# Performance work log

Measured on AMD Instinct MI355X. Metric: run time of the kernel, lower is better.

The kernel has to match this reference:

```python
import jax, jax.numpy as jnp
import numpy as np

KSIZE, STRIDE, RATE, FUSE_K, SCALE = 3, 1, 2, 3, 10.0
ESCAPE_NAN = 1e-4


def same_pad(x, k, s):
    # torch same_padding: pad so out = ceil(in/s)
    H, W = x.shape[2], x.shape[3]
    oh, ow = -(-H // s), -(-W // s)
    ph = max(0, (oh - 1) * s + k - H)
    pw = max(0, (ow - 1) * s + k - W)
    return jnp.pad(x, ((0, 0), (0, 0), (ph // 2, ph - ph // 2), (pw // 2, pw - pw // 2)))


def extract_patches(x, k, s):
    # torch Unfold -> view(B,C,k,k,L) -> permute(0,4,1,2,3): returns [B, L, C, k, k]
    x = same_pad(x, k, s)
    B, C, H, W = x.shape
    oh, ow = (H - k) // s + 1, (W - k) // s + 1
    rows = jnp.arange(oh)[:, None] * s + jnp.arange(k)[None, :]
    cols = jnp.arange(ow)[:, None] * s + jnp.arange(k)[None, :]
    p = x[:, :, rows][:, :, :, :, cols]  # [B,C,oh,k,ow,k]
    return p.transpose(0, 2, 4, 1, 3, 5).reshape(B, oh * ow, C, k, k)


def conv1x1(x, w, b):
    return jnp.einsum('bchw,oc->bohw', x, w) + b[None, :, None, None]


def conv2d(x, w):
    return jax.lax.conv_general_dilated(x, w, (1, 1), 'VALID',
                                        dimension_numbers=('NCHW', 'OIHW', 'NCHW'))


def conv_transpose2d(x, w, stride, pad):
    # matches F.conv_transpose2d(x, w[Cin,Cout,k,k], stride, padding=pad)
    k = w.shape[2]
    wf = jnp.flip(w, (2, 3))
    return jax.lax.conv_general_dilated(x, wf, (1, 1), [(k - 1 - pad, k - 1 - pad)] * 2,
                                        lhs_dilation=(stride, stride),
                                        dimension_numbers=('NCHW', 'IOHW', 'NCHW'))


def global_attention(a, bm, c, wq, bq, wk, bk, wv, bv, gamma):
    # a,bm: [B,C,H,W]; c: [B,1,Hc,Wc]; mask scales score rows before softmax
    B, C, H, W = a.shape
    dr = c.shape[2] // H
    c = c[:, :, ::dr, ::dr]  # nearest downsample, matches F.interpolate(mode='nearest')
    q = conv1x1(a, wq, bq).reshape(B, C, H * W)
    k = conv1x1(bm, wk, bk).reshape(B, C, H * W)
    sim = jnp.einsum('bci,bcj->bij', q, k)  # [B,N,N]
    mv = c.reshape(B, H * W)
    attn = jax.nn.softmax(sim * mv[:, :, None], axis=-1)
    v = conv1x1(a, wv, bv).reshape(B, C, H * W)
    out = jnp.einsum('bcj,bij->bci', v, attn).reshape(B, C, H, W)
    return gamma * a * c + (1.0 - c) * out


def _forward(f, b, mask, fa, pa):
    B, C, H, W = b.shape
    kernel = 2 * RATE
    raw_w = extract_patches(b, kernel, RATE * STRIDE)  # [B, L, C, 4, 4]
    f_ds = f[:, :, ::RATE, ::RATE]
    b_ds = b[:, :, ::RATE, ::RATE]
    Hd, Wd = f_ds.shape[2], f_ds.shape[3]
    mask0 = mask[0:1]  # torch uses m_groups[0] for all samples
    dr = mask0.shape[2] // Hd
    mask_ds = mask0[:, :, ::dr, ::dr]  # [1,1,Hd,Wd]
    w = extract_patches(b_ds, KSIZE, STRIDE)   # [B, L, C, 3, 3]
    fw = extract_patches(f_ds, KSIZE, STRIDE)  # [B, L, C, 3, 3]
    m = extract_patches(mask_ds, KSIZE, STRIDE)[0]  # [L, 1, 3, 3]
    mm = (jnp.mean(m, axis=(1, 2, 3), keepdims=True) == 0.0).astype(f.dtype)
    mm = mm.transpose(1, 0, 2, 3)  # [1, L, 1, 1]
    fuse_w = jnp.eye(FUSE_K, dtype=f.dtype).reshape(1, 1, FUSE_K, FUSE_K)

    def per_sample(xi, bi, fi_p, wi_p, raw_wi):
        # patch-level attention refines the dynamic conv kernels
        fp_p = global_attention(fi_p, wi_p, m, *pa)  # [L, C, 3, 3]
        norm = jnp.sqrt(jnp.sum(fp_p * fp_p, axis=(1, 2, 3), keepdims=True))
        wi_n = fp_p / jnp.maximum(norm, ESCAPE_NAN)
        # feature-level attention on the downsampled foreground
        fp = global_attention(xi[None], bi[None], mask_ds, *fa)  # [1,C,Hd,Wd]
        yi = conv2d(same_pad(fp, KSIZE, 1), wi_n)  # [1, L, Hd, Wd]
        Nb = Hd * Wd
        # fuse: identity-kernel smoothing over (bg-pos, fg-pos) score plane, twice
        yi = yi.reshape(1, 1, Nb, Nb)
        yi = conv2d(same_pad(yi, FUSE_K, 1), fuse_w)
        yi = yi.reshape(1, Hd, Wd, Hd, Wd).transpose(0, 2, 1, 4, 3).reshape(1, 1, Nb, Nb)
        yi = conv2d(same_pad(yi, FUSE_K, 1), fuse_w)
        yi = yi.reshape(1, Wd, Hd, Wd, Hd).transpose(0, 2, 1, 4, 3)
        yi = yi.reshape(1, Nb, Hd, Wd)
        yi = jax.nn.softmax(yi * mm * SCALE, axis=1) * mm
        return conv_transpose2d(yi, raw_wi, RATE, 1)[0] / 4.0  # [C, H, W]

    return jax.vmap(per_sample)(f_ds, b_ds, fw, w, raw_w)


def setup_inputs() -> dict:
    key = jax.random.key(0)
    ks = jax.random.split(key, 10)
    B, C, H, W = 2, 64, 96, 96
    f = jax.random.normal(ks[0], (B, C, H, W), jnp.float32)
    b = jax.random.normal(ks[1], (B, C, H, W), jnp.float32)
    mask = (jax.random.uniform(ks[2], (B, 1, H, W)) < 0.25).astype(jnp.float32)

    def wmat(k):
        return jax.random.normal(k, (C, C), jnp.float32) * 0.05

    return {
        'f': f, 'b': b, 'mask': mask,
        'fa_wq': wmat(ks[3]), 'fa_bq': jnp.zeros((C,), jnp.float32),
        'fa_wk': wmat(ks[4]), 'fa_bk': jnp.zeros((C,), jnp.float32),
        'fa_wv': wmat(ks[5]), 'fa_bv': jnp.zeros((C,), jnp.float32),
        'fa_gamma': jnp.ones((1,), jnp.float32),
        'pa_wq': wmat(ks[6]), 'pa_bq': jnp.zeros((C,), jnp.float32),
        'pa_wk': wmat(ks[7]), 'pa_bk': jnp.zeros((C,), jnp.float32),
        'pa_wv': wmat(ks[8]), 'pa_bv': jnp.zeros((C,), jnp.float32),
        'pa_gamma': jnp.ones((1,), jnp.float32),
    }


def reference(f, b, mask, fa_wq, fa_bq, fa_wk, fa_bk, fa_wv, fa_bv, fa_gamma,
              pa_wq, pa_bq, pa_wk, pa_bk, pa_wv, pa_bv, pa_gamma):
    fa = (fa_wq, fa_bq, fa_wk, fa_bk, fa_wv, fa_bv, fa_gamma)
    pa = (pa_wq, pa_bq, pa_wk, pa_bk, pa_wv, pa_bv, pa_gamma)
    return _forward(f, b, mask, fa, pa)
```

## Files before the change

### kernel.cpp

```cpp
#include <hip/hip_runtime.h>
#include <math.h>

#define HD 48
#define NB 2304
#define NC 64
#define IMG 96
#define NP 2401
#define KP 2432

#define CDIV(a,b) (((a)+(b)-1)/(b))

typedef unsigned short u16;
typedef __attribute__((ext_vector_type(8))) short  s16x8;
typedef __attribute__((ext_vector_type(8))) unsigned short u16x8;
typedef __attribute__((ext_vector_type(4))) float  f32x4;

constexpr size_t O_MASKDS = 0;
constexpr size_t O_MMP    = NB;
constexpr size_t O_CMAX   = (size_t)2*NB;
constexpr size_t O_CINV   = (size_t)4*NB;
constexpr size_t O_PMAX   = (size_t)6*NB;
constexpr size_t O_PSUM   = (size_t)38*NB;
constexpr size_t O_MEAN   = (size_t)70*NB;
constexpr size_t O_ACT    = (size_t)70*NB + 256;
constexpr size_t O_ROWIDX = O_ACT + 2434/1 + 62;
constexpr size_t O_INVROW = O_ROWIDX + 2560;
constexpr size_t O_NROW   = O_INVROW + NB;
constexpr size_t O_NEEDX  = O_NROW + 64;
constexpr size_t O_ARENA0 = O_NEEDX + NB + 64;
constexpr size_t A_FDS  = 0;
constexpr size_t A_FDST = 147456;
constexpr size_t A_SCR  = 294912;
constexpr size_t A_P0   = A_SCR + 2654208;
constexpr size_t A_P1   = A_P0 + (size_t)NB*NB;
constexpr size_t A_Y    = A_P1 + 5839232;
constexpr size_t A_B4   = A_Y + (size_t)NB*NB;
constexpr size_t SSTR   = A_B4 + 622592;
constexpr size_t TOTAL_F = O_ARENA0 + 2*SSTR;

__device__ inline void split_bf16(float x, u16& hi, u16& lo){
  unsigned int u = __float_as_uint(x);
  unsigned int r = u + 0x7FFFu + ((u >> 16) & 1u);
  hi = (u16)(r >> 16);
  float xh = __uint_as_float(((unsigned int)hi) << 16);
  float res = x - xh;
  unsigned int u2 = __float_as_uint(res);
  unsigned int r2 = u2 + 0x7FFFu + ((u2 >> 16) & 1u);
  lo = (u16)(r2 >> 16);
}


__global__ void k_prep_mask(const float* __restrict__ mask, float* __restrict__ maskds,
                            float* __restrict__ mmP){
  int q = blockIdx.x*256 + threadIdx.x;
  if(q >= NB) return;
  int hq = q/HD, wq = q%HD;
  maskds[q] = mask[(2*hq)*IMG + 2*wq];
  float any = 0.f;
  for(int u=-1;u<=1;u++)
    for(int v=-1;v<=1;v++){
      int y=hq+u, x=wq+v;
      if(y>=0&&y<HD&&x>=0&&x<HD) any += mask[(2*y)*IMG + 2*x];
    }
  mmP[wq*HD + hq] = (any == 0.f) ? 1.f : 0.f;
}

__global__ void k_actlist(const float* __restrict__ mmP, int* __restrict__ actIdx,
                          int* __restrict__ nActPad){
  __shared__ int cnt[256], base[256];
  int tid = threadIdx.x;
  int c0 = tid*10, c1 = min(c0+10, NP);
  int flags = 0, lc = 0;
  for(int i=c0;i<c1;i++){
    int ph=i/49, pw=i%49;
    bool act=false;
    #pragma unroll
    for(int a=0;a<2;a++)
      #pragma unroll
      for(int bb=0;bb<2;bb++){
        int sh=ph-a, sw=pw-bb;
        if(sh>=0&&sh<HD&&sw>=0&&sw<HD && mmP[sw*HD+sh]!=0.f) act=true;
      }
    if(act){ flags |= 1<<(i-c0); lc++; }
  }
  cnt[tid]=lc;
  __syncthreads();
  if(tid==0){
    int run=0;
    for(int i=0;i<256;i++){ base[i]=run; run+=cnt[i]; }
    int pad=(run+63)&~63;
    nActPad[0]=pad; nActPad[1]=run;
    for(int k=run;k<pad;k++) actIdx[k]=NP;
  }
  __syncthreads();
  int o=base[tid];
  for(int i=c0;i<c1;i++) if(flags & (1<<(i-c0))) actIdx[o++]=i;
}

__global__ void k_rowlist(const float* __restrict__ mmP, int* __restrict__ rowIdx,
                          int* __restrict__ invRow, int* __restrict__ nRowPad,
                          float* __restrict__ needXf){
  __shared__ unsigned char needX[NB], needS[NB];
  __shared__ int cnt[256], base[256];
  int tid = threadIdx.x;
  for(int i=tid;i<NB;i+=256){ needX[i]=0; }
  __syncthreads();
  for(int qp=tid; qp<NB; qp+=256){
    if(mmP[qp]!=0.f){
      #pragma unroll
      for(int d=-1;d<=1;d++){
        int rb=qp+d; if(rb<0||rb>=NB) continue;
        int b2=rb/HD, a=rb%HD;
        needX[a*HD + b2] = 1;
      }
    }
  }
  __syncthreads();
  for(int r=tid;r<NB;r+=256){
    unsigned char v = needX[r];
    if(r>0)    v |= needX[r-1];
    if(r<NB-1) v |= needX[r+1];
    needS[r]=v;
  }
  __syncthreads();
  int c0 = tid*9, c1 = min(c0+9, NB);
  int lc=0; for(int i=c0;i<c1;i++) lc += needS[i];
  cnt[tid]=lc;
  __syncthreads();
  if(tid==0){
    int run=0;
    for(int i=0;i<256;i++){ base[i]=run; run+=cnt[i]; }
    int pad=(run+127)&~127;
    nRowPad[0]=pad; nRowPad[1]=run;
    for(int k=run;k<pad;k++) rowIdx[k]=NB;
  }
  __syncthreads();
  int o=base[tid];
  for(int i=c0;i<c1;i++){
    if(needS[i]){ rowIdx[o]=i; invRow[i]=o; o++; }
    else invRow[i] = -1;
  }
  for(int i=tid;i<NB;i+=256) needXf[i] = needX[i] ? 1.f : 0.f;
}

__global__ void k_ds(const float* __restrict__ src, float* __restrict__ fds0,
                     float* __restrict__ fdsT0){
  int s = blockIdx.y;
  float* fds  = fds0  + (size_t)s*SSTR;
  float* fdsT = fdsT0 + (size_t)s*SSTR;
  int idx = blockIdx.x*256 + threadIdx.x;
  if(idx >= NC*NB) return;
  int c = idx/NB, j = idx%NB;
  int h = j/HD, w = j%HD;
  float v = src[(((size_t)s*NC + c)*IMG + 2*h)*IMG + 2*w];
  fds[idx] = v;
  fdsT[(size_t)j*64 + c] = v;
}

__global__ void k_colmean(const float* __restrict__ fds0, float* __restrict__ meanf){
  int s = blockIdx.y;
  const float* fds = fds0 + (size_t)s*SSTR;
  int c = blockIdx.x;
  int tid = threadIdx.x;
  float sum = 0.f;
  for(int j=tid; j<NB; j+=256) sum += fds[(size_t)c*NB + j];
  for(int off=32; off>0; off>>=1) sum += __shfl_down(sum, off);
  __shared__ float red[4];
  if((tid&63)==0) red[tid>>6] = sum;
  __syncthreads();
  if(tid==0) meanf[s*64 + c] = (red[0]+red[1]+red[2]+red[3]) * (1.f/NB);
}

__global__ void k_meanvf(const float* __restrict__ meanf, const float* __restrict__ wv,
                         const float* __restrict__ bv, float* __restrict__ meanVf){
  int s = blockIdx.x;
  __shared__ float mf[64];
  int c = threadIdx.x;
  mf[c] = meanf[s*64 + c];
  __syncthreads();
  float sum = 0.f;
  for(int cc=0;cc<64;cc++) sum += wv[c*64+cc]*mf[cc];
  meanVf[s*64 + c] = sum + bv[c];
}

__global__ void k_stageA(const float* __restrict__ fdsT0, const float* __restrict__ maskds,
                         const float* __restrict__ wv, const float* __restrict__ bv,
                         const float* __restrict__ gammap,
                         u16* __restrict__ AH0, u16* __restrict__ AL0){
  int s = blockIdx.y;
  const float* fdsT = fdsT0 + (size_t)s*SSTR;
  u16* AH = AH0 + (size_t)s*2*SSTR;
  u16* AL = AL0 + (size_t)s*2*SSTR;
  __shared__ float sumA[4][64];
  __shared__ float mval[4][9];
  int wsl = threadIdx.x>>6;
  int c = threadIdx.x&63;
  int p = blockIdx.x*4 + wsl;
  int ph = p/HD, pw = p%HD;
  float A[9]; float sa = 0.f;
  #pragma unroll
  for(int i=0;i<9;i++){
    int u=i/3, v=i%3;
    int y=ph+u-1, x=pw+v-1;
    bool in = (y>=0&&y<HD&&x>=0&&x<HD);
    float fv = in ? fdsT[(size_t)(y*HD+x)*64 + c] : 0.f;
    A[i] = fv; sa += fv;
    if(c==0) mval[wsl][i] = in ? maskds[y*HD+x] : 0.f;
  }
  sumA[wsl][c] = sa;
  __syncthreads();
  float acc = 0.f;
  for(int cc=0;cc<64;cc++) acc += wv[c*64+cc]*sumA[wsl][cc];
  float meanVc = acc*(1.f/9.f) + bv[c];
  float gamma = gammap[0];
  float fpv[9]; float ss = 0.f;
  #pragma unroll
  for(int i=0;i<9;i++){
    float v = (mval[wsl][i]!=0.f) ? gamma*A[i] : meanVc;
    fpv[i] = v; ss += v*v;
  }
  for(int off=32; off>0; off>>=1) ss += __shfl_down(ss, off);
  ss = __shfl(ss, 0);
  float scale = 1.f / fmaxf(sqrtf(ss), 1e-4f);
  #pragma unroll
  for(int i=0;i<9;i++){
    u16 h,l; split_bf16(fpv[i]*scale, h, l);
    size_t o = (size_t)p*576 + c*9 + i;
    AH[o] = h; AL[o] = l;
  }
}

__global__ void k_bcolT_split(const float* __restrict__ fds0, const float* __restrict__ maskds,
                              const float* __restrict__ meanVf, const float* __restrict__ gfp,
                              u16* __restrict__ BTH0, u16* __restrict__ BTL0){
  int s = blockIdx.y;
  const float* fds = fds0 + (size_t)s*SSTR;
  u16* BTH = BTH0 + (size_t)s*2*SSTR;
  u16* BTL = BTL0 + (size_t)s*2*SSTR;
  int idx = blockIdx.x*256 + threadIdx.x;
  if(idx >= NB*576) return;
  int P = idx/576, k = idx%576;
  int c = k/9, i = k%9, u = i/3, v = i%3;
  int hP = P/HD, wP = P%HD;
  int y = hP+u-1, x = wP+v-1;
  float val = 0.f;
  if(y>=0&&y<HD&&x>=0&&x<HD){
    int pos = y*HD + x;
    val = (maskds[pos]!=0.f) ? gfp[0]*fds[(size_t)c*NB + pos] : meanVf[s*64 + c];
  }
  u16 h,l; split_bf16(val, h, l);
  BTH[idx] = h; BTL[idx] = l;
}

__global__ __launch_bounds__(256, 2)
void k_gemm3(const u16* __restrict__ AH0, const u16* __restrict__ AL0,
             const u16* __restrict__ BTH0, const u16* __restrict__ BTL0,
             float* __restrict__ C0, int M, int N, int Kparam, int nz,
             const int* __restrict__ Kdev,
             const int* __restrict__ rowIdx, const int* __restrict__ Mdev,
             int ldA, int ldB, int ldC, long zstrC){
  __shared__ u16 sAH[2][128*32], sAL[2][128*32], sBH[2][128*32], sBL[2][128*32];
  int tid = threadIdx.x;
  int s = blockIdx.z / nz, zk = blockIdx.z % nz;
  int Mout = Mdev ? Mdev[0] : M;
  int m0 = blockIdx.y*128, n0 = blockIdx.x*128;
  if(m0 >= Mout) return;
  const u16* AH  = AH0  + (size_t)s*2*SSTR;
  const u16* AL  = AL0  + (size_t)s*2*SSTR;
  const u16* BTH = BTH0 + (size_t)s*2*SSTR;
  const u16* BTL = BTL0 + (size_t)s*2*SSTR;
  float* Cz = C0 + (size_t)s*SSTR + (size_t)zk*zstrC;
  int K = Kdev ? Kdev[0] : Kparam;
  int Kc = (((K+31)/32 + nz - 1)/nz)*32;
  int kbeg = zk*Kc; int kend = kbeg+Kc; if(kend>K) kend=K;
  int w = tid>>6, lane = tid&63;
  int wr = w>>1, wc = w&1;
  int fr = lane&15, fq = lane>>4;
  int r = tid>>1, hf = tid&1;
  int arow = m0+r;
  if(rowIdx) arow = rowIdx[arow];
  int br = n0+r;
  bool aok = (arow < M), bok = (br < N);
  int g0 = hf*2, g1 = hf*2+1;

  f32x4 acc[4][4];
  #pragma unroll
  for(int i=0;i<4;i++)
    #pragma unroll
    for(int j=0;j<4;j++) acc[i][j] = (f32x4){0.f,0.f,0.f,0.f};

  u16x8 pa0h,pa0l,pb0h,pb0l,pa1h,pa1l,pb1h,pb1l;
  const u16x8 z8 = (u16x8)(u16)0;

#define GLOAD(K0) { \
    pa0h=z8;pa0l=z8;pb0h=z8;pb0l=z8;pa1h=z8;pa1l=z8;pb1h=z8;pb1l=z8; \
    if(aok){ size_t o=(size_t)arow*ldA + (K0); \
      pa0h=*(const u16x8*)&AH[o+g0*8]; pa0l=*(const u16x8*)&AL[o+g0*8]; \
      pa1h=*(const u16x8*)&AH[o+g1*8]; pa1l=*(const u16x8*)&AL[o+g1*8]; } \
    if(bok){ size_t o=(size_t)br*ldB + (K0); \
      pb0h=*(const u16x8*)&BTH[o+g0*8]; pb0l=*(const u16x8*)&BTL[o+g0*8]; \
      pb1h=*(const u16x8*)&BTH[o+g1*8]; pb1l=*(const u16x8*)&BTL[o+g1*8]; } }

#define LSTORE(BUF) { \
    int gs0=(g0^((r>>1)&3))*8, gs1=(g1^((r>>1)&3))*8; \
    *(u16x8*)&sAH[BUF][r*32+gs0]=pa0h; *(u16x8*)&sAL[BUF][r*32+gs0]=pa0l; \
    *(u16x8*)&sBH[BUF][r*32+gs0]=pb0h; *(u16x8*)&sBL[BUF][r*32+gs0]=pb0l; \
    *(u16x8*)&sAH[BUF][r*32+gs1]=pa1h; *(u16x8*)&sAL[BUF][r*32+gs1]=pa1l; \
    *(u16x8*)&sBH[BUF][r*32+gs1]=pb1h; *(u16x8*)&sBL[BUF][r*32+gs1]=pb1l; }

  if(kbeg < kend){
    GLOAD(kbeg);
    LSTORE(0);
    if(kbeg+32 < kend) GLOAD(kbeg+32);
  }
  __syncthreads();
  int cur = 0;
  for(int k0=kbeg; k0<kend; k0+=32){
    if(k0+32 < kend){
      LSTORE(cur^1);
      if(k0+64 < kend) GLOAD(k0+64);
    }
    s16x8 a_h[4],a_l[4],b_h[4],b_l[4];
    #pragma unroll
    for(int mi=0;mi<4;mi++){
      int row=wr*64+mi*16+fr; int gs=(fq^((row>>1)&3))*8;
      a_h[mi]=*(const s16x8*)&sAH[cur][row*32+gs];
      a_l[mi]=*(const s16x8*)&sAL[cur][row*32+gs];
    }
    #pragma unroll
    for(int ni=0;ni<4;ni++){
      int row=wc*64+ni*16+fr; int gs=(fq^((row>>1)&3))*8;
      b_h[ni]=*(const s16x8*)&sBH[cur][row*32+gs];
      b_l[ni]=*(const s16x8*)&sBL[cur][row*32+gs];
    }
    #pragma unroll
    for(int mi=0;mi<4;mi++)
      #pragma unroll
      for(int ni=0;ni<4;ni++){
        acc[mi][ni] = __builtin_amdgcn_mfma_f32_16x16x32_bf16(a_h[mi], b_h[ni], acc[mi][ni], 0,0,0);
        acc[mi][ni] = __builtin_amdgcn_mfma_f32_16x16x32_bf16(a_h[mi], b_l[ni], acc[mi][ni], 0,0,0);
        acc[mi][ni] = __builtin_amdgcn_mfma_f32_16x16x32_bf16(a_l[mi], b_h[ni], acc[mi][ni], 0,0,0);
      }
    __syncthreads();
    cur ^= 1;
  }
#undef GLOAD
#undef LSTORE
  #pragma unroll
  for(int mi=0;mi<4;mi++)
    #pragma unroll
    for(int ni=0;ni<4;ni++){
      int row = m0 + wr*64 + mi*16 + fq*4;
      int col = n0 + wc*64 + ni*16 + fr;
      if(col < N){
        #pragma unroll
        for(int rr=0;rr<4;rr++)
          if(row+rr < Mout) Cz[(size_t)(row+rr)*ldC + col] = acc[mi][ni][rr];
      }
    }
}

__global__ void k_fuseP(const float* __restrict__ Sb, const int* __restrict__ invRow,
                        const float* __restrict__ needXf, float* __restrict__ Yb){
  int s = blockIdx.y;
  int r = blockIdx.x;
  if(needXf[r] == 0.f) return;
  const float* S = Sb + (size_t)s*SSTR;
  float* Y = Yb + (size_t)s*SSTR;
  int i0 = invRow[r];
  int im = (r>0)    ? invRow[r-1] : -1;
  int ip = (r<NB-1) ? invRow[r+1] : -1;
  __shared__ float lds[48*49];
  const float* row0 = S + (size_t)i0*NB;
  for(int t=threadIdx.x; t<NB; t+=256){
    float v = row0[t];
    if(im>=0 && t>0)    v += S[(size_t)im*NB + t-1];
    if(ip>=0 && t<NB-1) v += S[(size_t)ip*NB + t+1];
    lds[(t/HD)*49 + (t%HD)] = v;
  }
  __syncthreads();
  int a = r/HD, b2 = r%HD;
  float* orow = Y + (size_t)(b2*HD + a)*NB;
  for(int t=threadIdx.x; t<NB; t+=256){
    int d = t/HD, c = t%HD;
    orow[t] = lds[c*49 + d];
  }
}

__global__ void k_fuse_colsm(const float* __restrict__ Yb, const float* __restrict__ mmP,
                             float* __restrict__ pmax, float* __restrict__ psum){
  int s = blockIdx.z;
  const float* Y = Yb + (size_t)s*SSTR;
  int col = blockIdx.x*256 + threadIdx.x;
  int q0 = blockIdx.y*144;
  float mx = -1e30f, sum = 0.f;
  for(int q=q0; q<q0+144; q++){
    if(mmP[q] == 0.f) continue;
    float L = Y[(size_t)q*NB + col];
    if(q>0 && col>0)       L += Y[(size_t)(q-1)*NB + col-1];
    if(q<NB-1 && col<NB-1) L += Y[(size_t)(q+1)*NB + col+1];
    L *= 10.f;
    if(L > mx){ sum *= __expf(mx - L); mx = L; }
    sum += __expf(L - mx);
  }
  pmax[(size_t)(s*16 + blockIdx.y)*NB + col] = mx;
  psum[(size_t)(s*16 + blockIdx.y)*NB + col] = sum;
}

__global__ void k_combine(const float* __restrict__ pmax, const float* __restrict__ psum,
                          const float* __restrict__ mmP,
                          float* __restrict__ cmax, float* __restrict__ cinv){
  int s = blockIdx.y;
  int col = blockIdx.x*256 + threadIdx.x;
  int tid = threadIdx.x;
  __shared__ float redc[4];
  float cnt = 0.f;
  for(int k=tid; k<NB; k+=256) cnt += mmP[k];
  for(int off=32; off>0; off>>=1) cnt += __shfl_down(cnt, off);
  if((tid&63)==0) redc[tid>>6] = cnt;
  __syncthreads();
  float nAct = redc[0]+redc[1]+redc[2]+redc[3];
  float M = -1e30f;
  for(int k=0;k<16;k++) M = fmaxf(M, pmax[(size_t)(s*16+k)*NB + col]);
  if(nAct < NB - 0.5f) M = fmaxf(M, 0.f);
  float S = 0.f;
  for(int k=0;k<16;k++){
    float pm = pmax[(size_t)(s*16+k)*NB + col];
    float ps = psum[(size_t)(s*16+k)*NB + col];
    S += ps * __expf(pm - M);
  }
  S += ((float)NB - nAct) * __expf(0.f - M);
  cmax[s*NB + col] = M;
  cinv[s*NB + col] = 1.f/S;
}

__global__ void k_fuse_apply(const float* __restrict__ Yb, const float* __restrict__ mmP,
                             const float* __restrict__ cmax, const float* __restrict__ cinv,
                             float* __restrict__ yiTb){
  int s = blockIdx.y;
  const float* Y = Yb + (size_t)s*SSTR;
  float* yiT = yiTb + (size_t)s*SSTR;
  const float* cm = cmax + s*NB;
  const float* ci = cinv + s*NB;
  __shared__ float lds[48*49];
  int alpha = blockIdx.x/HD, delta = blockIdx.x%HD;
  for(int t=threadIdx.x; t<NB; t+=256){
    int beta = t/HD, gamma = t%HD;
    int qp = beta*HD + alpha;
    int Pp = delta*HD + gamma;
    float v = 0.f;
    if(mmP[qp] != 0.f){
      float L = Y[(size_t)qp*NB + Pp];
      if(qp>0 && Pp>0)       L += Y[(size_t)(qp-1)*NB + Pp-1];
      if(qp<NB-1 && Pp<NB-1) L += Y[(size_t)(qp+1)*NB + Pp+1];
      v = __expf(10.f*L - cm[Pp]) * ci[Pp];
    }
    lds[beta*49 + gamma] = v;
  }
  __syncthreads();
  for(int t=threadIdx.x; t<NB; t+=256){
    int gamma = t/HD, beta = t%HD;
    if(mmP[beta*HD + alpha] != 0.f)
      yiT[(size_t)(gamma*HD + delta)*NB + alpha*HD + beta] = lds[beta*49 + gamma];
  }
}

__global__ void k_zbuildT_split(const float* __restrict__ yiTb, const float* __restrict__ mmP,
                                const int* __restrict__ actIdx, const int* __restrict__ nActPad,
                                u16* __restrict__ UTH0, u16* __restrict__ UTL0){
  int s = blockIdx.z;
  const float* yiT = yiTb + (size_t)s*SSTR;
  u16* UTH = UTH0 + (size_t)s*2*SSTR;
  u16* UTL = UTL0 + (size_t)s*2*SSTR;
  int row = blockIdx.y;
  int cc  = blockIdx.x*256 + threadIdx.x;
  if(cc >= nActPad[0]) return;
  int pp = actIdx[cc];
  float z = 0.f;
  if(pp < NP){
    int rho = row/49, sig = row%49;
    int ph = pp/49, pw = pp%49;
    #pragma unroll
    for(int a=0;a<2;a++)
      #pragma unroll
      for(int bb=0;bb<2;bb++){
        int sh=ph-a, sw=pw-bb, rr=rho-a, ss=sig-bb;
        if(sh>=0 && sh<HD && sw>=0 && sw<HD && rr>=0 && rr<HD && ss>=0 && ss<HD
           && mmP[sw*HD+sh] != 0.f)
          z += yiT[(size_t)(rr*HD+ss)*NB + sh*HD+sw];
      }
  }
  u16 h,l; split_bf16(z, h, l);
  size_t o = (size_t)row*KP + cc;
  UTH[o] = h; UTL[o] = l;
}

__global__ void k_b4_split(const float* __restrict__ b,
                           const int* __restrict__ actIdx, const int* __restrict__ nActPad,
                           u16* __restrict__ B4H0, u16* __restrict__ B4L0){
  int s = blockIdx.y;
  u16* B4H = B4H0 + (size_t)s*2*SSTR;
  u16* B4L = B4L0 + (size_t)s*2*SSTR;
  int idx = blockIdx.x*256 + threadIdx.x;
  if(idx >= 256*KP) return;
  int m = idx/KP, kk = idx%KP;
  if(kk >= nActPad[0]) return;
  int pp = actIdx[kk];
  float val = 0.f;
  if(pp < NP){
    int phase = m>>6, c = m&63;
    int py = phase>>1, px = phase&1;
    int ph = pp/49, pw = pp%49;
    int y = 2*ph - py, x = 2*pw - px;
    if(y>=0&&y<IMG&&x>=0&&x<IMG) val = b[(((size_t)s*NC + c)*IMG + y)*IMG + x];
  }
  u16 h,l; split_bf16(val, h, l);
  B4H[idx] = h; B4L[idx] = l;
}

__global__ void k_epi(const float* __restrict__ Gb, float* __restrict__ out){
  int s = blockIdx.y;
  const float* G = Gb + (size_t)s*SSTR;
  int idx = blockIdx.x*256 + threadIdx.x;
  if(idx >= NC*IMG*IMG) return;
  int c = idx/(IMG*IMG), rem = idx%(IMG*IMG);
  int y = rem/IMG, x = rem%IMG;
  int py = y&1, px = x&1, r = y>>1, s2 = x>>1;
  size_t gi = (size_t)((py*2+px)*64 + c)*NP + (r+py)*49 + (s2+px);
  const size_t gz = (size_t)256*NP;
  float v = G[gi] + G[gi+gz] + G[gi+2*gz] + G[gi+3*gz];
  out[((size_t)s*NC + c)*IMG*IMG + rem] = v * 0.25f;
}

extern "C" void kernel_launch(void* const* d_in, const int* in_sizes, int n_in,
                              void* d_out, int out_size, void* d_ws, size_t ws_size,
                              hipStream_t stream){
  const float* f    = (const float*)d_in[0];
  const float* b    = (const float*)d_in[1];
  const float* mask = (const float*)d_in[2];
  const float* fa_wv=(const float*)d_in[7];  const float* fa_bv=(const float*)d_in[8];
  const float* fa_g =(const float*)d_in[9];
  const float* pa_wv=(const float*)d_in[14]; const float* pa_bv=(const float*)d_in[15];
  const float* pa_g =(const float*)d_in[16];
  float* out = (float*)d_out;
  float* ws  = (float*)d_ws;
  if(ws_size < TOTAL_F*sizeof(float)) return;

  float* maskds = ws + O_MASKDS;
  float* mmP    = ws + O_MMP;
  float* cmax   = ws + O_CMAX;
  float* cinv   = ws + O_CINV;
  float* pmax   = ws + O_PMAX;
  float* psum   = ws + O_PSUM;
  float* meanf  = ws + O_MEAN;
  float* meanVf = ws + O_MEAN + 128;
  int*   actIdx  = (int*)(ws + O_ACT);
  int*   nActPad = actIdx + 2432;
  int*   rowIdx  = (int*)(ws + O_ROWIDX);
  int*   invRow  = (int*)(ws + O_INVROW);
  int*   nRowPad = (int*)(ws + O_NROW);
  float* needXf  = ws + O_NEEDX;

  float* fds0  = ws + O_ARENA0 + A_FDS;
  float* fdsT0 = ws + O_ARENA0 + A_FDST;
  u16*   AH0   = (u16*)(ws + O_ARENA0 + A_SCR);
  u16*   AL0   = AH0 + (size_t)NB*576;
  u16*   BTH0  = AL0 + (size_t)NB*576;
  u16*   BTL0  = BTH0 + (size_t)NB*576;
  float* G0    = ws + O_ARENA0 + A_SCR;
  float* Scmp0 = ws + O_ARENA0 + A_P0;
  float* Y0    = ws + O_ARENA0 + A_Y;
  float* yiT0  = Scmp0;
  u16*   UTH0  = (u16*)(ws + O_ARENA0 + A_P1);
  u16*   UTL0  = UTH0 + (size_t)NP*KP;
  u16*   B4H0  = (u16*)(ws + O_ARENA0 + A_B4);
  u16*   B4L0  = B4H0 + (size_t)256*KP;

  k_prep_mask<<<9, 256, 0, stream>>>(mask, maskds, mmP);
  k_actlist<<<1, 256, 0, stream>>>(mmP, actIdx, nActPad);
  k_rowlist<<<1, 256, 0, stream>>>(mmP, rowIdx, invRow, nRowPad, needXf);
  k_ds<<<dim3(CDIV(NC*NB,256), 2), 256, 0, stream>>>(f, fds0, fdsT0);
  k_colmean<<<dim3(64, 2), 256, 0, stream>>>(fds0, meanf);
  k_meanvf<<<2, 64, 0, stream>>>(meanf, fa_wv, fa_bv, meanVf);
  k_stageA<<<dim3(NB/4, 2), 256, 0, stream>>>(fdsT0, maskds, pa_wv, pa_bv, pa_g, AH0, AL0);
  k_bcolT_split<<<dim3(CDIV(NB*576,256), 2), 256, 0, stream>>>(fds0, maskds, meanVf, fa_g, BTH0, BTL0);

  k_gemm3<<<dim3(18,18,2), 256, 0, stream>>>(AH0, AL0, BTH0, BTL0, Scmp0,
      NB, NB, 576, 1, nullptr, rowIdx, nRowPad, 576, 576, NB, 0L);

  k_fuseP<<<dim3(NB, 2), 256, 0, stream>>>(Scmp0, invRow, needXf, Y0);
  k_fuse_colsm<<<dim3(9,16,2), 256, 0, stream>>>(Y0, mmP, pmax, psum);
  k_combine<<<dim3(9, 2), 256, 0, stream>>>(pmax, psum, mmP, cmax, cinv);
  k_fuse_apply<<<dim3(NB, 2), 256, 0, stream>>>(Y0, mmP, cmax, cinv, yiT0);

  k_zbuildT_split<<<dim3(CDIV(KP,256), NP, 2), 256, 0, stream>>>(yiT0, mmP, actIdx, nActPad, UTH0, UTL0);
  k_b4_split<<<dim3(CDIV(256*KP,256), 2), 256, 0, stream>>>(b, actIdx, nActPad, B4H0, B4L0);
  k_gemm3<<<dim3(CDIV(NP,128), 2, 8), 256, 0, stream>>>(B4H0, B4L0, UTH0, UTL0, G0,
      256, NP, KP, 4, nActPad, nullptr, nullptr, KP, KP, NP, (long)256*NP);
  k_epi<<<dim3(CDIV(NC*IMG*IMG,256), 2), 256, 0, stream>>>(G0, out);
}
```

Baseline: 224.1 us.

## Use direct global-to-LDS loads in GEMM, swizzle blocks across XCDs, merge prep kernels

The split-bf16 GEMM now issues global_load_lds 16-byte copies straight into shared memory instead of staging tiles through registers. Invalid rows read from a zero pad buffer. Workgroup IDs are remapped so neighbouring tiles land on the same XCD for better L2 reuse. Three tiny single-purpose prep kernels are merged into one launch that keeps the mask in LDS. This cuts register pressure and launch overhead, at the cost of a smaller prefetch distance (one stage instead of register double-buffering) and a single-block prep kernel.

```diff
diff --git a/kernel.cpp b/kernel.cpp
--- a/kernel.cpp
+++ b/kernel.cpp
@@ -27,6 +27,7 @@
 constexpr size_t O_INVROW = O_ROWIDX + 2560;
 constexpr size_t O_NROW   = O_INVROW + NB;
 constexpr size_t O_NEEDX  = O_NROW + 64;
+constexpr size_t O_ZPAD   = O_NEEDX + NB;
 constexpr size_t O_ARENA0 = O_NEEDX + NB + 64;
 constexpr size_t A_FDS  = 0;
 constexpr size_t A_FDST = 147456;
@@ -49,98 +50,107 @@
   lo = (u16)(r2 >> 16);
 }
 
-
-__global__ void k_prep_mask(const float* __restrict__ mask, float* __restrict__ maskds,
-                            float* __restrict__ mmP){
-  int q = blockIdx.x*256 + threadIdx.x;
-  if(q >= NB) return;
-  int hq = q/HD, wq = q%HD;
-  maskds[q] = mask[(2*hq)*IMG + 2*wq];
-  float any = 0.f;
-  for(int u=-1;u<=1;u++)
-    for(int v=-1;v<=1;v++){
-      int y=hq+u, x=wq+v;
-      if(y>=0&&y<HD&&x>=0&&x<HD) any += mask[(2*y)*IMG + 2*x];
-    }
-  mmP[wq*HD + hq] = (any == 0.f) ? 1.f : 0.f;
-}
-
-__global__ void k_actlist(const float* __restrict__ mmP, int* __restrict__ actIdx,
-                          int* __restrict__ nActPad){
-  __shared__ int cnt[256], base[256];
-  int tid = threadIdx.x;
-  int c0 = tid*10, c1 = min(c0+10, NP);
-  int flags = 0, lc = 0;
-  for(int i=c0;i<c1;i++){
-    int ph=i/49, pw=i%49;
-    bool act=false;
-    #pragma unroll
-    for(int a=0;a<2;a++)
-      #pragma unroll
-      for(int bb=0;bb<2;bb++){
-        int sh=ph-a, sw=pw-bb;
-        if(sh>=0&&sh<HD&&sw>=0&&sw<HD && mmP[sw*HD+sh]!=0.f) act=true;
-      }
-    if(act){ flags |= 1<<(i-c0); lc++; }
-  }
-  cnt[tid]=lc;
-  __syncthreads();
-  if(tid==0){
-    int run=0;
-    for(int i=0;i<256;i++){ base[i]=run; run+=cnt[i]; }
-    int pad=(run+63)&~63;
-    nActPad[0]=pad; nActPad[1]=run;
-    for(int k=run;k<pad;k++) actIdx[k]=NP;
-  }
-  __syncthreads();
-  int o=base[tid];
-  for(int i=c0;i<c1;i++) if(flags & (1<<(i-c0))) actIdx[o++]=i;
-}
-
-__global__ void k_rowlist(const float* __restrict__ mmP, int* __restrict__ rowIdx,
-                          int* __restrict__ invRow, int* __restrict__ nRowPad,
-                          float* __restrict__ needXf){
+__device__ __forceinline__ void gload16(const u16* g, u16* l){
+  __builtin_amdgcn_global_load_lds(
+      (const __attribute__((address_space(1))) unsigned int*)g,
+      (__attribute__((address_space(3))) unsigned int*)l, 16, 0, 0);
+}
+
+
+__global__ void k_prep(const float* __restrict__ mask, float* __restrict__ maskds,
+                       float* __restrict__ mmP,
+                       int* __restrict__ actIdx, int* __restrict__ nActPad,
+                       int* __restrict__ rowIdx, int* __restrict__ invRow,
+                       int* __restrict__ nRowPad, float* __restrict__ needXf,
+                       u16* __restrict__ zp){
+  __shared__ float lmm[NB];
   __shared__ unsigned char needX[NB], needS[NB];
   __shared__ int cnt[256], base[256];
   int tid = threadIdx.x;
-  for(int i=tid;i<NB;i+=256){ needX[i]=0; }
-  __syncthreads();
-  for(int qp=tid; qp<NB; qp+=256){
-    if(mmP[qp]!=0.f){
+  for(int q=tid; q<NB; q+=256){
+    int hq = q/HD, wq = q%HD;
+    maskds[q] = mask[(2*hq)*IMG + 2*wq];
+    float any = 0.f;
+    for(int u=-1;u<=1;u++)
+      for(int v=-1;v<=1;v++){
+        int y=hq+u, x=wq+v;
+        if(y>=0&&y<HD&&x>=0&&x<HD) any += mask[(2*y)*IMG + 2*x];
+      }
+    float v = (any == 0.f) ? 1.f : 0.f;
+    mmP[wq*HD + hq] = v;
+    lmm[wq*HD + hq] = v;
+  }
+  if(tid < 16) ((unsigned int*)zp)[tid] = 0u;
+  __syncthreads();
+  {
+    int c0 = tid*10, c1 = min(c0+10, NP);
+    int flags = 0, lc = 0;
+    for(int i=c0;i<c1;i++){
+      int ph=i/49, pw=i%49;
+      bool act=false;
       #pragma unroll
-      for(int d=-1;d<=1;d++){
-        int rb=qp+d; if(rb<0||rb>=NB) continue;
-        int b2=rb/HD, a=rb%HD;
-        needX[a*HD + b2] = 1;
+      for(int a=0;a<2;a++)
+        #pragma unroll
+        for(int bb=0;bb<2;bb++){
+          int sh=ph-a, sw=pw-bb;
+          if(sh>=0&&sh<HD&&sw>=0&&sw<HD && lmm[sw*HD+sh]!=0.f) act=true;
+        }
+      if(act){ flags |= 1<<(i-c0); lc++; }
+    }
+    cnt[tid]=lc;
+    __syncthreads();
+    if(tid==0){
+      int run=0;
+      for(int i=0;i<256;i++){ base[i]=run; run+=cnt[i]; }
+      int pad=(run+63)&~63;
+      nActPad[0]=pad; nActPad[1]=run;
+      for(int k=run;k<pad;k++) actIdx[k]=NP;
+    }
+    __syncthreads();
+    int o=base[tid];
+    for(int i=c0;i<c1;i++) if(flags & (1<<(i-c0))) actIdx[o++]=i;
+  }
+  __syncthreads();
+  {
+    for(int i=tid;i<NB;i+=256) needX[i]=0;
+    __syncthreads();
+    for(int qp=tid; qp<NB; qp+=256){
+      if(lmm[qp]!=0.f){
+        #pragma unroll
+        for(int d=-1;d<=1;d++){
+          int rb=qp+d; if(rb<0||rb>=NB) continue;
+          int b2=rb/HD, a=rb%HD;
+          needX[a*HD + b2] = 1;
+        }
       }
     }
-  }
-  __syncthreads();
-  for(int r=tid;r<NB;r+=256){
-    unsigned char v = needX[r];
-    if(r>0)    v |= needX[r-1];
-    if(r<NB-1) v |= needX[r+1];
-    needS[r]=v;
-  }
-  __syncthreads();
-  int c0 = tid*9, c1 = min(c0+9, NB);
-  int lc=0; for(int i=c0;i<c1;i++) lc += needS[i];
-  cnt[tid]=lc;
-  __syncthreads();
-  if(tid==0){
-    int run=0;
-    for(int i=0;i<256;i++){ base[i]=run; run+=cnt[i]; }
-    int pad=(run+127)&~127;
-    nRowPad[0]=pad; nRowPad[1]=run;
-    for(int k=run;k<pad;k++) rowIdx[k]=NB;
-  }
-  __syncthreads();
-  int o=base[tid];
-  for(int i=c0;i<c1;i++){
-    if(needS[i]){ rowIdx[o]=i; invRow[i]=o; o++; }
-    else invRow[i] = -1;
-  }
-  for(int i=tid;i<NB;i+=256) needXf[i] = needX[i] ? 1.f : 0.f;
+    __syncthreads();
+    for(int r=tid;r<NB;r+=256){
+      unsigned char v = needX[r];
+      if(r>0)    v |= needX[r-1];
+      if(r<NB-1) v |= needX[r+1];
+      needS[r]=v;
+    }
+    __syncthreads();
+    int c0 = tid*9, c1 = min(c0+9, NB);
+    int lc=0; for(int i=c0;i<c1;i++) lc += needS[i];
+    cnt[tid]=lc;
+    __syncthreads();
+    if(tid==0){
+      int run=0;
+      for(int i=0;i<256;i++){ base[i]=run; run+=cnt[i]; }
+      int pad=(run+127)&~127;
+      nRowPad[0]=pad; nRowPad[1]=run;
+      for(int k=run;k<pad;k++) rowIdx[k]=NB;
+    }
+    __syncthreads();
+    int o=base[tid];
+    for(int i=c0;i<c1;i++){
+      if(needS[i]){ rowIdx[o]=i; invRow[i]=o; o++; }
+      else invRow[i] = -1;
+    }
+    for(int i=tid;i<NB;i+=256) needXf[i] = needX[i] ? 1.f : 0.f;
+  }
 }
 
 __global__ void k_ds(const float* __restrict__ src, float* __restrict__ fds0,
@@ -253,17 +263,25 @@
 }
 
 __global__ __launch_bounds__(256, 2)
-void k_gemm3(const u16* __restrict__ AH0, const u16* __restrict__ AL0,
+void k_gemm4(const u16* __restrict__ AH0, const u16* __restrict__ AL0,
              const u16* __restrict__ BTH0, const u16* __restrict__ BTL0,
              float* __restrict__ C0, int M, int N, int Kparam, int nz,
              const int* __restrict__ Kdev,
              const int* __restrict__ rowIdx, const int* __restrict__ Mdev,
+             const u16* __restrict__ zp,
              int ldA, int ldB, int ldC, long zstrC){
   __shared__ u16 sAH[2][128*32], sAL[2][128*32], sBH[2][128*32], sBL[2][128*32];
   int tid = threadIdx.x;
   int s = blockIdx.z / nz, zk = blockIdx.z % nz;
   int Mout = Mdev ? Mdev[0] : M;
-  int m0 = blockIdx.y*128, n0 = blockIdx.x*128;
+  int gx = gridDim.x;
+  int nwg = gx*gridDim.y;
+  int orig = blockIdx.y*gx + blockIdx.x;
+  int xcd = orig & 7;
+  int qq = nwg>>3, rr2 = nwg&7;
+  int swz = (xcd<rr2 ? xcd*(qq+1) : rr2*(qq+1) + (xcd-rr2)*qq) + (orig>>3);
+  int by = swz/gx, bx = swz - by*gx;
+  int m0 = by*128, n0 = bx*128;
   if(m0 >= Mout) return;
   const u16* AH  = AH0  + (size_t)s*2*SSTR;
   const u16* AL  = AL0  + (size_t)s*2*SSTR;
@@ -276,12 +294,37 @@
   int w = tid>>6, lane = tid&63;
   int wr = w>>1, wc = w&1;
   int fr = lane&15, fq = lane>>4;
-  int r = tid>>1, hf = tid&1;
-  int arow = m0+r;
-  if(rowIdx) arow = rowIdx[arow];
-  int br = n0+r;
-  bool aok = (arow < M), bok = (br < N);
-  int g0 = hf*2, g1 = hf*2+1;
+
+  int ch0 = w, ch1 = 4+w;
+  int rl0 = ch0*16 + (lane>>2), rl1 = ch1*16 + (lane>>2);
+  int gp = lane&3;
+  int gr0 = (gp ^ ((rl0>>1)&3))*8;
+  int gr1 = (gp ^ ((rl1>>1)&3))*8;
+  int mi0 = m0+rl0, mi1 = m0+rl1;
+  int ar0 = rowIdx ? rowIdx[mi0] : mi0;
+  int ar1 = rowIdx ? rowIdx[mi1] : mi1;
+  bool av0 = (ar0 < M), av1 = (ar1 < M);
+  int br0 = n0+rl0, br1 = n0+rl1;
+  bool bv0 = (br0 < N), bv1 = (br1 < N);
+  const u16* pAH0 = AH + (size_t)(av0?ar0:0)*ldA + gr0;
+  const u16* pAH1 = AH + (size_t)(av1?ar1:0)*ldA + gr1;
+  const u16* pAL0 = AL + (size_t)(av0?ar0:0)*ldA + gr0;
+  const u16* pAL1 = AL + (size_t)(av1?ar1:0)*ldA + gr1;
+  const u16* pBH0 = BTH + (size_t)(bv0?br0:0)*ldB + gr0;
+  const u16* pBH1 = BTH + (size_t)(bv1?br1:0)*ldB + gr1;
+  const u16* pBL0 = BTL + (size_t)(bv0?br0:0)*ldB + gr0;
+  const u16* pBL1 = BTL + (size_t)(bv1?br1:0)*ldB + gr1;
+  int lo0 = ch0*512, lo1 = ch1*512;
+
+#define GISSUE(BUF, K0) { \
+    gload16(av0 ? pAH0+(K0) : zp, &sAH[BUF][lo0]); \
+    gload16(av1 ? pAH1+(K0) : zp, &sAH[BUF][lo1]); \
+    gload16(av0 ? pAL0+(K0) : zp, &sAL[BUF][lo0]); \
+    gload16(av1 ? pAL1+(K0) : zp, &sAL[BUF][lo1]); \
+    gload16(bv0 ? pBH0+(K0) : zp, &sBH[BUF][lo0]); \
+    gload16(bv1 ? pBH1+(K0) : zp, &sBH[BUF][lo1]); \
+    gload16(bv0 ? pBL0+(K0) : zp, &sBL[BUF][lo0]); \
+    gload16(bv1 ? pBL1+(K0) : zp, &sBL[BUF][lo1]); }
 
   f32x4 acc[4][4];
   #pragma unroll
@@ -289,37 +332,11 @@
     #pragma unroll
     for(int j=0;j<4;j++) acc[i][j] = (f32x4){0.f,0.f,0.f,0.f};
 
-  u16x8 pa0h,pa0l,pb0h,pb0l,pa1h,pa1l,pb1h,pb1l;
-  const u16x8 z8 = (u16x8)(u16)0;
-
-#define GLOAD(K0) { \
-    pa0h=z8;pa0l=z8;pb0h=z8;pb0l=z8;pa1h=z8;pa1l=z8;pb1h=z8;pb1l=z8; \
-    if(aok){ size_t o=(size_t)arow*ldA + (K0); \
-      pa0h=*(const u16x8*)&AH[o+g0*8]; pa0l=*(const u16x8*)&AL[o+g0*8]; \
-      pa1h=*(const u16x8*)&AH[o+g1*8]; pa1l=*(const u16x8*)&AL[o+g1*8]; } \
-    if(bok){ size_t o=(size_t)br*ldB + (K0); \
-      pb0h=*(const u16x8*)&BTH[o+g0*8]; pb0l=*(const u16x8*)&BTL[o+g0*8]; \
-      pb1h=*(const u16x8*)&BTH[o+g1*8]; pb1l=*(const u16x8*)&BTL[o+g1*8]; } }
-
-#define LSTORE(BUF) { \
-    int gs0=(g0^((r>>1)&3))*8, gs1=(g1^((r>>1)&3))*8; \
-    *(u16x8*)&sAH[BUF][r*32+gs0]=pa0h; *(u16x8*)&sAL[BUF][r*32+gs0]=pa0l; \
-    *(u16x8*)&sBH[BUF][r*32+gs0]=pb0h; *(u16x8*)&sBL[BUF][r*32+gs0]=pb0l; \
-    *(u16x8*)&sAH[BUF][r*32+gs1]=pa1h; *(u16x8*)&sAL[BUF][r*32+gs1]=pa1l; \
-    *(u16x8*)&sBH[BUF][r*32+gs1]=pb1h; *(u16x8*)&sBL[BUF][r*32+gs1]=pb1l; }
-
-  if(kbeg < kend){
-    GLOAD(kbeg);
-    LSTORE(0);
-    if(kbeg+32 < kend) GLOAD(kbeg+32);
-  }
+  if(kbeg < kend){ GISSUE(0, kbeg); }
   __syncthreads();
   int cur = 0;
   for(int k0=kbeg; k0<kend; k0+=32){
-    if(k0+32 < kend){
-      LSTORE(cur^1);
-      if(k0+64 < kend) GLOAD(k0+64);
-    }
+    if(k0+32 < kend) GISSUE(cur^1, k0+32);
     s16x8 a_h[4],a_l[4],b_h[4],b_l[4];
     #pragma unroll
     for(int mi=0;mi<4;mi++){
@@ -344,8 +361,7 @@
     __syncthreads();
     cur ^= 1;
   }
-#undef GLOAD
-#undef LSTORE
+#undef GISSUE
   #pragma unroll
   for(int mi=0;mi<4;mi++)
     #pragma unroll
@@ -560,6 +576,7 @@
   int*   invRow  = (int*)(ws + O_INVROW);
   int*   nRowPad = (int*)(ws + O_NROW);
   float* needXf  = ws + O_NEEDX;
+  u16*   zp      = (u16*)(ws + O_ZPAD);
 
   float* fds0  = ws + O_ARENA0 + A_FDS;
   float* fdsT0 = ws + O_ARENA0 + A_FDST;
@@ -576,17 +593,16 @@
   u16*   B4H0  = (u16*)(ws + O_ARENA0 + A_B4);
   u16*   B4L0  = B4H0 + (size_t)256*KP;
 
-  k_prep_mask<<<9, 256, 0, stream>>>(mask, maskds, mmP);
-  k_actlist<<<1, 256, 0, stream>>>(mmP, actIdx, nActPad);
-  k_rowlist<<<1, 256, 0, stream>>>(mmP, rowIdx, invRow, nRowPad, needXf);
+  k_prep<<<1, 256, 0, stream>>>(mask, maskds, mmP, actIdx, nActPad,
+                                rowIdx, invRow, nRowPad, needXf, zp);
   k_ds<<<dim3(CDIV(NC*NB,256), 2), 256, 0, stream>>>(f, fds0, fdsT0);
   k_colmean<<<dim3(64, 2), 256, 0, stream>>>(fds0, meanf);
   k_meanvf<<<2, 64, 0, stream>>>(meanf, fa_wv, fa_bv, meanVf);
   k_stageA<<<dim3(NB/4, 2), 256, 0, stream>>>(fdsT0, maskds, pa_wv, pa_bv, pa_g, AH0, AL0);
   k_bcolT_split<<<dim3(CDIV(NB*576,256), 2), 256, 0, stream>>>(fds0, maskds, meanVf, fa_g, BTH0, BTL0);
 
-  k_gemm3<<<dim3(18,18,2), 256, 0, stream>>>(AH0, AL0, BTH0, BTL0, Scmp0,
-      NB, NB, 576, 1, nullptr, rowIdx, nRowPad, 576, 576, NB, 0L);
+  k_gemm4<<<dim3(18,18,2), 256, 0, stream>>>(AH0, AL0, BTH0, BTL0, Scmp0,
+      NB, NB, 576, 1, nullptr, rowIdx, nRowPad, zp, 576, 576, NB, 0L);
 
   k_fuseP<<<dim3(NB, 2), 256, 0, stream>>>(Scmp0, invRow, needXf, Y0);
   k_fuse_colsm<<<dim3(9,16,2), 256, 0, stream>>>(Y0, mmP, pmax, psum);
@@ -595,7 +611,7 @@
 
   k_zbuildT_split<<<dim3(CDIV(KP,256), NP, 2), 256, 0, stream>>>(yiT0, mmP, actIdx, nActPad, UTH0, UTL0);
   k_b4_split<<<dim3(CDIV(256*KP,256), 2), 256, 0, stream>>>(b, actIdx, nActPad, B4H0, B4L0);
-  k_gemm3<<<dim3(CDIV(NP,128), 2, 8), 256, 0, stream>>>(B4H0, B4L0, UTH0, UTL0, G0,
-      256, NP, KP, 4, nActPad, nullptr, nullptr, KP, KP, NP, (long)256*NP);
+  k_gemm4<<<dim3(CDIV(NP,128), 2, 8), 256, 0, stream>>>(B4H0, B4L0, UTH0, UTL0, G0,
+      256, NP, KP, 4, nActPad, nullptr, nullptr, zp, KP, KP, NP, (long)256*NP);
   k_epi<<<dim3(CDIV(NC*IMG*IMG,256), 2), 256, 0, stream>>>(G0, out);
 }
```

Measured after the change: 224.9 us. About the same (+0.4%).
